# Performance work log

Hardware: AMD Instinct MI355X
Metric: run time of the kernel (lower is better)

Reference implementation:

```python
import jax, jax.numpy as jnp
import numpy as np

N_NODES = 50000
N_EDGES = 800000
IN_DIM, HID_DIM, OUT_DIM, N_HEADS = 256, 256, 64, 4

def setup_inputs() -> dict:
    key = jax.random.key(0)
    ks = jax.random.split(key, 8)
    x = jax.random.normal(ks[0], (N_NODES, IN_DIM), dtype=jnp.float32)
    idx = jax.random.randint(ks[1], (2, N_EDGES), 0, N_NODES, dtype=jnp.int64)
    elem = jax.random.uniform(ks[2], (N_EDGES,), dtype=jnp.float32)
    # MLP params (2 layers: in->hid, hid->out), one set per head; small scale for stability
    W1 = jax.random.normal(ks[3], (N_HEADS, IN_DIM, HID_DIM), dtype=jnp.float32) * 0.05
    b1 = jnp.zeros((N_HEADS, HID_DIM), dtype=jnp.float32)
    W2 = jax.random.normal(ks[4], (N_HEADS, HID_DIM, OUT_DIM), dtype=jnp.float32) * 0.05
    b2 = jnp.zeros((N_HEADS, OUT_DIM), dtype=jnp.float32)
    # Attention: Linear(2*out+1 -> 1)
    attn_w = jax.random.normal(ks[5], (N_HEADS, 2 * OUT_DIM + 1, 1), dtype=jnp.float32) * 0.05
    attn_b = jnp.zeros((N_HEADS, 1), dtype=jnp.float32)
    return {"x": x, "idx": idx, "elem": elem, "W1": W1, "b1": b1,
            "W2": W2, "b2": b2, "attn_w": attn_w, "attn_b": attn_b}

def reference(x, idx, elem, W1, b1, W2, b2, attn_w, attn_b):
    n = x.shape[0]
    src, dst = idx[0], idx[1]

    def head(W1h, b1h, W2h, b2h, awh, abh):
        # 2-layer MLP on node features: [N, out]
        feats = jnp.maximum(x @ W1h + b1h, 0.0) @ W2h + b2h
        f_src = feats[src]            # [E, out]
        f_dst = feats[dst]            # [E, out]
        x_cat = jnp.concatenate([f_src, f_dst, elem[:, None]], axis=1)  # [E, 2*out+1]
        score = (x_cat @ awh + abh)[:, 0]                # [E]
        w = jnp.exp(score - jnp.max(score))              # globally-shifted exp, as in source
        # SpecialSpmm: sparse [N,N] (rows=src, cols=dst, vals=w) @ dense
        pooled = jax.ops.segment_sum(w[:, None] * f_dst, src, num_segments=n)  # [N, out]
        row_sum = jax.ops.segment_sum(w, src, num_segments=n)                  # [N]
        return pooled / row_sum[:, None]

    h = jax.vmap(head)(W1, b1, W2, b2, attn_w, attn_b)   # [H, N, out]
    return jnp.transpose(h, (1, 0, 2)).reshape(n, -1)    # cat heads -> [N, H*out]
```

## Files before the change

### kernel.cpp

```cpp
#include <hip/hip_runtime.h>
#include <math.h>


#define N_HEADS 4
#define IN_DIM 256
#define HID_DIM 256
#define OUT_DIM 64
#define ATT_STRIDE (2 * OUT_DIM + 1)
#define LDSP 264

typedef __attribute__((ext_vector_type(8))) short bf16x8;
typedef __attribute__((ext_vector_type(4))) float f32x4;

__device__ __forceinline__ unsigned short bf16rne(float f) {
  unsigned int u = __float_as_uint(f);
  u += 0x7fffu + ((u >> 16) & 1u);
  return (unsigned short)(u >> 16);
}


#define W1N (N_HEADS * IN_DIM * HID_DIM)
#define W2N (N_HEADS * HID_DIM * OUT_DIM)

__global__ __launch_bounds__(256) void convw_kernel(const float* __restrict__ W1,
                                                    const float* __restrict__ W2,
                                                    unsigned short* __restrict__ W1T,
                                                    unsigned short* __restrict__ W2T) {
  int id = blockIdx.x * 256 + threadIdx.x;
  if (id < W1N) {
    int k = id & 255, j = (id >> 8) & 255, h = id >> 16;
    W1T[id] = bf16rne(W1[((size_t)h * 256 + k) * 256 + j]);
  } else if (id < W1N + W2N) {
    int t = id - W1N;
    int k = t & 255, d = (t >> 8) & 63, h = t >> 14;
    W2T[t] = bf16rne(W2[((size_t)h * 256 + k) * 64 + d]);
  }
}


__global__ __launch_bounds__(256) void count_kernel(const int* __restrict__ src,
                                                    int* __restrict__ cnt, int E) {
  int e = blockIdx.x * 256 + threadIdx.x;
  if (e < E) atomicAdd(&cnt[src[e]], 1);
}

__global__ __launch_bounds__(1024) void scan_kernel(const int* __restrict__ cnt,
                                                    int* __restrict__ offs, int N) {
  __shared__ int part[1024];
  int t = threadIdx.x;
  int chunk = (N + 1023) >> 10;
  int s0 = t * chunk;
  int s1e = min(s0 + chunk, N);
  int sum = 0;
  for (int i = s0; i < s1e; ++i) sum += cnt[i];
  part[t] = sum;
  __syncthreads();
  for (int off = 1; off < 1024; off <<= 1) {
    int v = (t >= off) ? part[t - off] : 0;
    __syncthreads();
    part[t] += v;
    __syncthreads();
  }
  int run = (t == 0) ? 0 : part[t - 1];
  for (int i = s0; i < s1e; ++i) { offs[i] = run; run += cnt[i]; }
  if (t == 0) offs[N] = part[1023];
}

__global__ __launch_bounds__(256) void scatter_kernel(
    const int* __restrict__ src, const int* __restrict__ dst,
    const float* __restrict__ elem, const int* __restrict__ offs,
    int* __restrict__ cur, int* __restrict__ dst2, float* __restrict__ elem2,
    int E) {
  int e = blockIdx.x * 256 + threadIdx.x;
  if (e < E) {
    int s = src[e];
    int pos = offs[s] + atomicAdd(&cur[s], 1);
    dst2[pos] = dst[e];
    elem2[pos] = elem[e];
  }
}


__global__ __launch_bounds__(256) void feats_kernel(
    const float* __restrict__ x, const unsigned short* __restrict__ W1T,
    const float* __restrict__ b1, const unsigned short* __restrict__ W2T,
    const float* __restrict__ b2, const float* __restrict__ attn_w,
    const float* __restrict__ attn_b, float* __restrict__ feats,
    float* __restrict__ s1, float* __restrict__ s2, int N) {
  __shared__ __align__(16) unsigned short xs[64 * LDSP];
  __shared__ __align__(16) unsigned short hs[64 * LDSP];

  int h = blockIdx.y;
  int n0 = blockIdx.x * 64;
  int tid = threadIdx.x;
  int w = tid >> 6, l = tid & 63;
  int lr = l & 15, kb = l >> 4;

#pragma unroll
  for (int i = 0; i < 8; ++i) {
    int flat = i * 2048 + tid * 8;
    int r = flat >> 8, c = flat & 255;
    int n = n0 + r;
    float4 v0 = make_float4(0.f, 0.f, 0.f, 0.f), v1 = v0;
    if (n < N) {
      const float* p = x + (size_t)n * IN_DIM + c;
      v0 = *(const float4*)p;
      v1 = *(const float4*)(p + 4);
    }
    uint4 pk;
    pk.x = (unsigned)bf16rne(v0.x) | ((unsigned)bf16rne(v0.y) << 16);
    pk.y = (unsigned)bf16rne(v0.z) | ((unsigned)bf16rne(v0.w) << 16);
    pk.z = (unsigned)bf16rne(v1.x) | ((unsigned)bf16rne(v1.y) << 16);
    pk.w = (unsigned)bf16rne(v1.z) | ((unsigned)bf16rne(v1.w) << 16);
    *(uint4*)&xs[r * LDSP + c] = pk;
  }
  __syncthreads();

  int j0 = w * 64;
  const unsigned short* W1Th = W1T + (size_t)h * 256 * 256;
  f32x4 acc[4][4];
#pragma unroll
  for (int mi = 0; mi < 4; ++mi)
#pragma unroll
    for (int ni = 0; ni < 4; ++ni) acc[mi][ni] = (f32x4){0.f, 0.f, 0.f, 0.f};

#pragma unroll
  for (int kk = 0; kk < 8; ++kk) {
    int k0 = kk * 32 + kb * 8;
    bf16x8 a[4], b[4];
#pragma unroll
    for (int mi = 0; mi < 4; ++mi)
      a[mi] = *(const bf16x8*)&xs[(mi * 16 + lr) * LDSP + k0];
#pragma unroll
    for (int ni = 0; ni < 4; ++ni)
      b[ni] = *(const bf16x8*)(W1Th + (size_t)(j0 + ni * 16 + lr) * 256 + k0);
#pragma unroll
    for (int mi = 0; mi < 4; ++mi)
#pragma unroll
      for (int ni = 0; ni < 4; ++ni)
        acc[mi][ni] = __builtin_amdgcn_mfma_f32_16x16x32_bf16(a[mi], b[ni],
                                                              acc[mi][ni], 0, 0, 0);
  }

  float b1v[4];
#pragma unroll
  for (int ni = 0; ni < 4; ++ni) b1v[ni] = b1[h * HID_DIM + j0 + ni * 16 + lr];
#pragma unroll
  for (int mi = 0; mi < 4; ++mi)
#pragma unroll
    for (int ni = 0; ni < 4; ++ni)
#pragma unroll
      for (int r = 0; r < 4; ++r) {
        float v = fmaxf(acc[mi][ni][r] + b1v[ni], 0.0f);
        hs[(mi * 16 + kb * 4 + r) * LDSP + (j0 + ni * 16 + lr)] = bf16rne(v);
      }
  __syncthreads();

  const unsigned short* W2Th = W2T + (size_t)h * 64 * 256;
  f32x4 acc2[4];
#pragma unroll
  for (int ni = 0; ni < 4; ++ni) acc2[ni] = (f32x4){0.f, 0.f, 0.f, 0.f};
#pragma unroll
  for (int kk = 0; kk < 8; ++kk) {
    int k0 = kk * 32 + kb * 8;
    bf16x8 a = *(const bf16x8*)&hs[(w * 16 + lr) * LDSP + k0];
#pragma unroll
    for (int ni = 0; ni < 4; ++ni) {
      bf16x8 b = *(const bf16x8*)(W2Th + (size_t)(ni * 16 + lr) * 256 + k0);
      acc2[ni] = __builtin_amdgcn_mfma_f32_16x16x32_bf16(a, b, acc2[ni], 0, 0, 0);
    }
  }

  const float* awh = attn_w + h * ATT_STRIDE;
  float a1v[4], a2v[4], b2v[4];
#pragma unroll
  for (int ni = 0; ni < 4; ++ni) {
    int d = ni * 16 + lr;
    a1v[ni] = awh[d];
    a2v[ni] = awh[OUT_DIM + d];
    b2v[ni] = b2[h * OUT_DIM + d];
  }
#pragma unroll
  for (int r = 0; r < 4; ++r) {
    int n = n0 + w * 16 + kb * 4 + r;
    float vals[4];
    float p1 = 0.f, p2 = 0.f;
#pragma unroll
    for (int ni = 0; ni < 4; ++ni) {
      float v = acc2[ni][r] + b2v[ni];
      vals[ni] = v;
      p1 += v * a1v[ni];
      p2 += v * a2v[ni];
    }
#pragma unroll
    for (int m = 1; m < 16; m <<= 1) {
      p1 += __shfl_xor(p1, m, 64);
      p2 += __shfl_xor(p2, m, 64);
    }
    if (n < N) {
      float* fr = feats + ((size_t)h * N + n) * OUT_DIM;
#pragma unroll
      for (int ni = 0; ni < 4; ++ni) fr[ni * 16 + lr] = vals[ni];
      if (lr == 0) {
        s1[(size_t)h * N + n] = p1;
        s2[(size_t)h * N + n] = p2;
      }
    }
  }
}


__global__ __launch_bounds__(256) void edgemax_kernel(
    const int* __restrict__ src, const int* __restrict__ dst,
    const float* __restrict__ elem, const float* __restrict__ s1,
    const float* __restrict__ s2, const float* __restrict__ attn_w,
    const float* __restrict__ attn_b, float* __restrict__ blockmax, int N, int E) {
  int e = blockIdx.x * 256 + threadIdx.x;
  float sc[N_HEADS];
  if (e < E) {
    int s = src[e], dn = dst[e];
    float el = elem[e];
#pragma unroll
    for (int h = 0; h < N_HEADS; ++h)
      sc[h] = s1[(size_t)h * N + s] + s2[(size_t)h * N + dn] +
              attn_w[h * ATT_STRIDE + 2 * OUT_DIM] * el + attn_b[h];
  } else {
#pragma unroll
    for (int h = 0; h < N_HEADS; ++h) sc[h] = -INFINITY;
  }
  __shared__ float wm[N_HEADS][4];
  int lane = threadIdx.x & 63, wv = threadIdx.x >> 6;
#pragma unroll
  for (int h = 0; h < N_HEADS; ++h) {
    float m = sc[h];
#pragma unroll
    for (int off = 32; off > 0; off >>= 1) m = fmaxf(m, __shfl_down(m, off, 64));
    if (lane == 0) wm[h][wv] = m;
  }
  __syncthreads();
  if (threadIdx.x < N_HEADS) {
    int h = threadIdx.x;
    float m = fmaxf(fmaxf(wm[h][0], wm[h][1]), fmaxf(wm[h][2], wm[h][3]));
    blockmax[blockIdx.x * N_HEADS + h] = m;
  }
}

__global__ __launch_bounds__(256) void reducemax_kernel(
    const float* __restrict__ blockmax, float* __restrict__ maxs, int nb) {
  __shared__ float red[256];
  int tid = threadIdx.x;
  for (int h = 0; h < N_HEADS; ++h) {
    float m = -INFINITY;
    for (int i = tid; i < nb; i += 256) m = fmaxf(m, blockmax[i * N_HEADS + h]);
    red[tid] = m;
    __syncthreads();
    for (int s = 128; s > 0; s >>= 1) {
      if (tid < s) red[tid] = fmaxf(red[tid], red[tid + s]);
      __syncthreads();
    }
    if (tid == 0) maxs[h] = red[0];
    __syncthreads();
  }
}


#define AGG_U 8

__global__ __launch_bounds__(256) void aggregate_kernel(
    const int* __restrict__ dst2, const float* __restrict__ elem2,
    const int* __restrict__ offs, const float* __restrict__ s1,
    const float* __restrict__ s2, const float* __restrict__ feats,
    const float* __restrict__ attn_w, const float* __restrict__ attn_b,
    const float* __restrict__ maxs, float* __restrict__ out, int N) {
  int n = blockIdx.x;
  int h = threadIdx.x >> 6, d = threadIdx.x & 63;
  int beg = offs[n], end = offs[n + 1];
  float s1n = s1[(size_t)h * N + n];
  float awe = attn_w[h * ATT_STRIDE + 2 * OUT_DIM];
  float ab = attn_b[h];
  float mx = maxs[h];
  const float* fh = feats + (size_t)h * N * OUT_DIM;
  const float* s2h = s2 + (size_t)h * N;
  float acc = 0.f, rs = 0.f;
  float base = s1n + ab - mx;

  for (int p = beg; p < end; p += AGG_U) {
    int dn[AGG_U];
    float el[AGG_U];
#pragma unroll
    for (int i = 0; i < AGG_U; ++i) {
      int q = (p + i < end) ? p + i : beg;
      dn[i] = dst2[q];
      el[i] = elem2[q];
    }
    float s2v[AGG_U], fv[AGG_U];
#pragma unroll
    for (int i = 0; i < AGG_U; ++i) s2v[i] = s2h[dn[i]];
#pragma unroll
    for (int i = 0; i < AGG_U; ++i) fv[i] = fh[(size_t)dn[i] * OUT_DIM + d];
#pragma unroll
    for (int i = 0; i < AGG_U; ++i) {
      float wv = (p + i < end) ? __expf(base + s2v[i] + awe * el[i]) : 0.f;
      acc = fmaf(wv, fv[i], acc);
      rs += wv;
    }
  }
  out[(size_t)n * (N_HEADS * OUT_DIM) + h * OUT_DIM + d] = acc / rs;
}


extern "C" void kernel_launch(void* const* d_in, const int* in_sizes, int n_in,
                              void* d_out, int out_size, void* d_ws, size_t ws_size,
                              hipStream_t stream) {
  const float* x = (const float*)d_in[0];
  const int* idx = (const int*)d_in[1];
  const float* elem = (const float*)d_in[2];
  const float* W1 = (const float*)d_in[3];
  const float* b1 = (const float*)d_in[4];
  const float* W2 = (const float*)d_in[5];
  const float* b2 = (const float*)d_in[6];
  const float* attn_w = (const float*)d_in[7];
  const float* attn_b = (const float*)d_in[8];
  float* out = (float*)d_out;

  int N = in_sizes[0] / IN_DIM;
  int E = in_sizes[2];
  const int* src = idx;
  const int* dst = idx + E;
  int nb = (E + 255) / 256;

  unsigned short* W1T = (unsigned short*)d_ws;
  unsigned short* W2T = W1T + W1N;
  float* feats = (float*)(W2T + W2N);
  float* s1 = feats + (size_t)N_HEADS * N * OUT_DIM;
  float* s2 = s1 + (size_t)N_HEADS * N;
  float* blockmax = s2 + (size_t)N_HEADS * N;
  float* maxs = blockmax + (size_t)nb * N_HEADS;
  int* offs = (int*)(maxs + 64);
  int* cur = offs + (N + 64);
  int* dst2 = cur + (N + 64);
  float* elem2 = (float*)(dst2 + E);

  convw_kernel<<<(W1N + W2N + 255) / 256, 256, 0, stream>>>(W1, W2, W1T, W2T);

  hipMemsetAsync(cur, 0, sizeof(int) * (size_t)N, stream);
  count_kernel<<<nb, 256, 0, stream>>>(src, cur, E);
  scan_kernel<<<1, 1024, 0, stream>>>(cur, offs, N);
  hipMemsetAsync(cur, 0, sizeof(int) * (size_t)N, stream);
  scatter_kernel<<<nb, 256, 0, stream>>>(src, dst, elem, offs, cur, dst2, elem2, E);

  dim3 g((N + 63) / 64, N_HEADS);
  feats_kernel<<<g, 256, 0, stream>>>(x, W1T, b1, W2T, b2, attn_w, attn_b,
                                      feats, s1, s2, N);
  edgemax_kernel<<<nb, 256, 0, stream>>>(src, dst, elem, s1, s2, attn_w, attn_b,
                                         blockmax, N, E);
  reducemax_kernel<<<1, 256, 0, stream>>>(blockmax, maxs, nb);
  aggregate_kernel<<<N, 256, 0, stream>>>(dst2, elem2, offs, s1, s2, feats,
                                          attn_w, attn_b, maxs, out, N);
}
```

Baseline: 565.1 us.

## Drop global max pass, store feats in bf16, loop heads per block

Removes the edge max and reduce-max kernels, relying on the cancellation of the global shift in the normalized softmax ratio. It stores node features as bf16 and s1/s2 node-major to halve the gather traffic in aggregation. Aggregation now processes two edges per wave, with each lane handling two feature elements, and combines the halves with a cross-lane shuffle. The feature kernel loops over all heads in one block so the x tile is loaded and converted once. Without the max shift, exp can overflow for large scores, and bf16 features reduce precision.

```diff
diff --git a/kernel.cpp b/kernel.cpp
--- a/kernel.cpp
+++ b/kernel.cpp
@@ -85,12 +85,11 @@
     const float* __restrict__ x, const unsigned short* __restrict__ W1T,
     const float* __restrict__ b1, const unsigned short* __restrict__ W2T,
     const float* __restrict__ b2, const float* __restrict__ attn_w,
-    const float* __restrict__ attn_b, float* __restrict__ feats,
-    float* __restrict__ s1, float* __restrict__ s2, int N) {
+    const float* __restrict__ attn_b, unsigned short* __restrict__ feats_g,
+    float* __restrict__ s1p, float* __restrict__ s2p, int N) {
   __shared__ __align__(16) unsigned short xs[64 * LDSP];
   __shared__ __align__(16) unsigned short hs[64 * LDSP];
 
-  int h = blockIdx.y;
   int n0 = blockIdx.x * 64;
   int tid = threadIdx.x;
   int w = tid >> 6, l = tid & 63;
@@ -117,149 +116,98 @@
   __syncthreads();
 
   int j0 = w * 64;
-  const unsigned short* W1Th = W1T + (size_t)h * 256 * 256;
-  f32x4 acc[4][4];
-#pragma unroll
-  for (int mi = 0; mi < 4; ++mi)
-#pragma unroll
-    for (int ni = 0; ni < 4; ++ni) acc[mi][ni] = (f32x4){0.f, 0.f, 0.f, 0.f};
-
-#pragma unroll
-  for (int kk = 0; kk < 8; ++kk) {
-    int k0 = kk * 32 + kb * 8;
-    bf16x8 a[4], b[4];
+  for (int h = 0; h < N_HEADS; ++h) {
+    const unsigned short* W1Th = W1T + (size_t)h * 256 * 256;
+    f32x4 acc[4][4];
 #pragma unroll
     for (int mi = 0; mi < 4; ++mi)
-      a[mi] = *(const bf16x8*)&xs[(mi * 16 + lr) * LDSP + k0];
-#pragma unroll
-    for (int ni = 0; ni < 4; ++ni)
-      b[ni] = *(const bf16x8*)(W1Th + (size_t)(j0 + ni * 16 + lr) * 256 + k0);
+#pragma unroll
+      for (int ni = 0; ni < 4; ++ni) acc[mi][ni] = (f32x4){0.f, 0.f, 0.f, 0.f};
+
+#pragma unroll
+    for (int kk = 0; kk < 8; ++kk) {
+      int k0 = kk * 32 + kb * 8;
+      bf16x8 a[4], b[4];
+#pragma unroll
+      for (int mi = 0; mi < 4; ++mi)
+        a[mi] = *(const bf16x8*)&xs[(mi * 16 + lr) * LDSP + k0];
+#pragma unroll
+      for (int ni = 0; ni < 4; ++ni)
+        b[ni] = *(const bf16x8*)(W1Th + (size_t)(j0 + ni * 16 + lr) * 256 + k0);
+#pragma unroll
+      for (int mi = 0; mi < 4; ++mi)
+#pragma unroll
+        for (int ni = 0; ni < 4; ++ni)
+          acc[mi][ni] = __builtin_amdgcn_mfma_f32_16x16x32_bf16(a[mi], b[ni],
+                                                                acc[mi][ni], 0, 0, 0);
+    }
+
+    float b1v[4];
+#pragma unroll
+    for (int ni = 0; ni < 4; ++ni) b1v[ni] = b1[h * HID_DIM + j0 + ni * 16 + lr];
+    __syncthreads();
 #pragma unroll
     for (int mi = 0; mi < 4; ++mi)
 #pragma unroll
       for (int ni = 0; ni < 4; ++ni)
-        acc[mi][ni] = __builtin_amdgcn_mfma_f32_16x16x32_bf16(a[mi], b[ni],
-                                                              acc[mi][ni], 0, 0, 0);
-  }
-
-  float b1v[4];
-#pragma unroll
-  for (int ni = 0; ni < 4; ++ni) b1v[ni] = b1[h * HID_DIM + j0 + ni * 16 + lr];
-#pragma unroll
-  for (int mi = 0; mi < 4; ++mi)
-#pragma unroll
-    for (int ni = 0; ni < 4; ++ni)
-#pragma unroll
-      for (int r = 0; r < 4; ++r) {
-        float v = fmaxf(acc[mi][ni][r] + b1v[ni], 0.0f);
-        hs[(mi * 16 + kb * 4 + r) * LDSP + (j0 + ni * 16 + lr)] = bf16rne(v);
+#pragma unroll
+        for (int r = 0; r < 4; ++r) {
+          float v = fmaxf(acc[mi][ni][r] + b1v[ni], 0.0f);
+          hs[(mi * 16 + kb * 4 + r) * LDSP + (j0 + ni * 16 + lr)] = bf16rne(v);
+        }
+    __syncthreads();
+
+    const unsigned short* W2Th = W2T + (size_t)h * 64 * 256;
+    f32x4 acc2[4];
+#pragma unroll
+    for (int ni = 0; ni < 4; ++ni) acc2[ni] = (f32x4){0.f, 0.f, 0.f, 0.f};
+#pragma unroll
+    for (int kk = 0; kk < 8; ++kk) {
+      int k0 = kk * 32 + kb * 8;
+      bf16x8 a = *(const bf16x8*)&hs[(w * 16 + lr) * LDSP + k0];
+#pragma unroll
+      for (int ni = 0; ni < 4; ++ni) {
+        bf16x8 b = *(const bf16x8*)(W2Th + (size_t)(ni * 16 + lr) * 256 + k0);
+        acc2[ni] = __builtin_amdgcn_mfma_f32_16x16x32_bf16(a, b, acc2[ni], 0, 0, 0);
       }
-  __syncthreads();
-
-  const unsigned short* W2Th = W2T + (size_t)h * 64 * 256;
-  f32x4 acc2[4];
-#pragma unroll
-  for (int ni = 0; ni < 4; ++ni) acc2[ni] = (f32x4){0.f, 0.f, 0.f, 0.f};
-#pragma unroll
-  for (int kk = 0; kk < 8; ++kk) {
-    int k0 = kk * 32 + kb * 8;
-    bf16x8 a = *(const bf16x8*)&hs[(w * 16 + lr) * LDSP + k0];
+    }
+
+    const float* awh = attn_w + h * ATT_STRIDE;
+    float a1v[4], a2v[4], b2v[4];
 #pragma unroll
     for (int ni = 0; ni < 4; ++ni) {
-      bf16x8 b = *(const bf16x8*)(W2Th + (size_t)(ni * 16 + lr) * 256 + k0);
-      acc2[ni] = __builtin_amdgcn_mfma_f32_16x16x32_bf16(a, b, acc2[ni], 0, 0, 0);
-    }
-  }
-
-  const float* awh = attn_w + h * ATT_STRIDE;
-  float a1v[4], a2v[4], b2v[4];
-#pragma unroll
-  for (int ni = 0; ni < 4; ++ni) {
-    int d = ni * 16 + lr;
-    a1v[ni] = awh[d];
-    a2v[ni] = awh[OUT_DIM + d];
-    b2v[ni] = b2[h * OUT_DIM + d];
-  }
-#pragma unroll
-  for (int r = 0; r < 4; ++r) {
-    int n = n0 + w * 16 + kb * 4 + r;
-    float vals[4];
-    float p1 = 0.f, p2 = 0.f;
-#pragma unroll
-    for (int ni = 0; ni < 4; ++ni) {
-      float v = acc2[ni][r] + b2v[ni];
-      vals[ni] = v;
-      p1 += v * a1v[ni];
-      p2 += v * a2v[ni];
-    }
-#pragma unroll
-    for (int m = 1; m < 16; m <<= 1) {
-      p1 += __shfl_xor(p1, m, 64);
-      p2 += __shfl_xor(p2, m, 64);
-    }
-    if (n < N) {
-      float* fr = feats + ((size_t)h * N + n) * OUT_DIM;
-#pragma unroll
-      for (int ni = 0; ni < 4; ++ni) fr[ni * 16 + lr] = vals[ni];
-      if (lr == 0) {
-        s1[(size_t)h * N + n] = p1;
-        s2[(size_t)h * N + n] = p2;
+      int d = ni * 16 + lr;
+      a1v[ni] = awh[d];
+      a2v[ni] = awh[OUT_DIM + d];
+      b2v[ni] = b2[h * OUT_DIM + d];
+    }
+#pragma unroll
+    for (int r = 0; r < 4; ++r) {
+      int n = n0 + w * 16 + kb * 4 + r;
+      float vals[4];
+      float p1 = 0.f, p2 = 0.f;
+#pragma unroll
+      for (int ni = 0; ni < 4; ++ni) {
+        float v = acc2[ni][r] + b2v[ni];
+        vals[ni] = v;
+        p1 += v * a1v[ni];
+        p2 += v * a2v[ni];
       }
-    }
-  }
-}
-
-
-__global__ __launch_bounds__(256) void edgemax_kernel(
-    const int* __restrict__ src, const int* __restrict__ dst,
-    const float* __restrict__ elem, const float* __restrict__ s1,
-    const float* __restrict__ s2, const float* __restrict__ attn_w,
-    const float* __restrict__ attn_b, float* __restrict__ blockmax, int N, int E) {
-  int e = blockIdx.x * 256 + threadIdx.x;
-  float sc[N_HEADS];
-  if (e < E) {
-    int s = src[e], dn = dst[e];
-    float el = elem[e];
-#pragma unroll
-    for (int h = 0; h < N_HEADS; ++h)
-      sc[h] = s1[(size_t)h * N + s] + s2[(size_t)h * N + dn] +
-              attn_w[h * ATT_STRIDE + 2 * OUT_DIM] * el + attn_b[h];
-  } else {
-#pragma unroll
-    for (int h = 0; h < N_HEADS; ++h) sc[h] = -INFINITY;
-  }
-  __shared__ float wm[N_HEADS][4];
-  int lane = threadIdx.x & 63, wv = threadIdx.x >> 6;
-#pragma unroll
-  for (int h = 0; h < N_HEADS; ++h) {
-    float m = sc[h];
-#pragma unroll
-    for (int off = 32; off > 0; off >>= 1) m = fmaxf(m, __shfl_down(m, off, 64));
-    if (lane == 0) wm[h][wv] = m;
-  }
-  __syncthreads();
-  if (threadIdx.x < N_HEADS) {
-    int h = threadIdx.x;
-    float m = fmaxf(fmaxf(wm[h][0], wm[h][1]), fmaxf(wm[h][2], wm[h][3]));
-    blockmax[blockIdx.x * N_HEADS + h] = m;
-  }
-}
-
-__global__ __launch_bounds__(256) void reducemax_kernel(
-    const float* __restrict__ blockmax, float* __restrict__ maxs, int nb) {
-  __shared__ float red[256];
-  int tid = threadIdx.x;
-  for (int h = 0; h < N_HEADS; ++h) {
-    float m = -INFINITY;
-    for (int i = tid; i < nb; i += 256) m = fmaxf(m, blockmax[i * N_HEADS + h]);
-    red[tid] = m;
-    __syncthreads();
-    for (int s = 128; s > 0; s >>= 1) {
-      if (tid < s) red[tid] = fmaxf(red[tid], red[tid + s]);
-      __syncthreads();
-    }
-    if (tid == 0) maxs[h] = red[0];
-    __syncthreads();
+#pragma unroll
+      for (int m = 1; m < 16; m <<= 1) {
+        p1 += __shfl_xor(p1, m, 64);
+        p2 += __shfl_xor(p2, m, 64);
+      }
+      if (n < N) {
+        unsigned short* fr = feats_g + ((size_t)h * N + n) * OUT_DIM;
+#pragma unroll
+        for (int ni = 0; ni < 4; ++ni) fr[ni * 16 + lr] = bf16rne(vals[ni]);
+        if (lr == 0) {
+          s1p[(size_t)n * N_HEADS + h] = p1;
+          s2p[(size_t)n * N_HEADS + h] = p2;
+        }
+      }
+    }
   }
 }
 
@@ -268,44 +216,55 @@
 
 __global__ __launch_bounds__(256) void aggregate_kernel(
     const int* __restrict__ dst2, const float* __restrict__ elem2,
-    const int* __restrict__ offs, const float* __restrict__ s1,
-    const float* __restrict__ s2, const float* __restrict__ feats,
+    const int* __restrict__ offs, const float* __restrict__ s1p,
+    const float* __restrict__ s2p, const unsigned short* __restrict__ feats_g,
     const float* __restrict__ attn_w, const float* __restrict__ attn_b,
-    const float* __restrict__ maxs, float* __restrict__ out, int N) {
+    float* __restrict__ out, int N) {
   int n = blockIdx.x;
-  int h = threadIdx.x >> 6, d = threadIdx.x & 63;
+  int h = threadIdx.x >> 6;
+  int l = threadIdx.x & 63;
+  int j = l >> 5, dp = l & 31;
   int beg = offs[n], end = offs[n + 1];
-  float s1n = s1[(size_t)h * N + n];
+  float base = s1p[(size_t)n * N_HEADS + h] + attn_b[h];
   float awe = attn_w[h * ATT_STRIDE + 2 * OUT_DIM];
-  float ab = attn_b[h];
-  float mx = maxs[h];
-  const float* fh = feats + (size_t)h * N * OUT_DIM;
-  const float* s2h = s2 + (size_t)h * N;
-  float acc = 0.f, rs = 0.f;
-  float base = s1n + ab - mx;
-
-  for (int p = beg; p < end; p += AGG_U) {
+  const unsigned short* fg = feats_g + (size_t)h * N * OUT_DIM;
+  float acc0 = 0.f, acc1 = 0.f, rs = 0.f;
+
+  for (int p = beg; p < end; p += 2 * AGG_U) {
     int dn[AGG_U];
     float el[AGG_U];
 #pragma unroll
     for (int i = 0; i < AGG_U; ++i) {
-      int q = (p + i < end) ? p + i : beg;
-      dn[i] = dst2[q];
-      el[i] = elem2[q];
-    }
-    float s2v[AGG_U], fv[AGG_U];
-#pragma unroll
-    for (int i = 0; i < AGG_U; ++i) s2v[i] = s2h[dn[i]];
-#pragma unroll
-    for (int i = 0; i < AGG_U; ++i) fv[i] = fh[(size_t)dn[i] * OUT_DIM + d];
+      int q = p + 2 * i + j;
+      int qq = (q < end) ? q : beg;
+      dn[i] = dst2[qq];
+      el[i] = elem2[qq];
+    }
+    float s2v[AGG_U];
+    unsigned int fv[AGG_U];
+#pragma unroll
+    for (int i = 0; i < AGG_U; ++i) s2v[i] = s2p[(size_t)dn[i] * N_HEADS + h];
+#pragma unroll
+    for (int i = 0; i < AGG_U; ++i)
+      fv[i] = *(const unsigned int*)&fg[(size_t)dn[i] * OUT_DIM + 2 * dp];
 #pragma unroll
     for (int i = 0; i < AGG_U; ++i) {
-      float wv = (p + i < end) ? __expf(base + s2v[i] + awe * el[i]) : 0.f;
-      acc = fmaf(wv, fv[i], acc);
+      float wv = (p + 2 * i + j < end) ? __expf(base + s2v[i] + awe * el[i]) : 0.f;
+      float f0 = __uint_as_float(fv[i] << 16);
+      float f1 = __uint_as_float(fv[i] & 0xffff0000u);
+      acc0 = fmaf(wv, f0, acc0);
+      acc1 = fmaf(wv, f1, acc1);
       rs += wv;
     }
   }
-  out[(size_t)n * (N_HEADS * OUT_DIM) + h * OUT_DIM + d] = acc / rs;
+  acc0 += __shfl_xor(acc0, 32, 64);
+  acc1 += __shfl_xor(acc1, 32, 64);
+  rs += __shfl_xor(rs, 32, 64);
+  if (j == 0) {
+    float inv = 1.0f / rs;
+    float2 o = make_float2(acc0 * inv, acc1 * inv);
+    *(float2*)&out[(size_t)n * (N_HEADS * OUT_DIM) + h * OUT_DIM + 2 * dp] = o;
+  }
 }
 
 
@@ -331,12 +290,10 @@
 
   unsigned short* W1T = (unsigned short*)d_ws;
   unsigned short* W2T = W1T + W1N;
-  float* feats = (float*)(W2T + W2N);
-  float* s1 = feats + (size_t)N_HEADS * N * OUT_DIM;
-  float* s2 = s1 + (size_t)N_HEADS * N;
-  float* blockmax = s2 + (size_t)N_HEADS * N;
-  float* maxs = blockmax + (size_t)nb * N_HEADS;
-  int* offs = (int*)(maxs + 64);
+  unsigned short* feats_g = W2T + W2N;
+  float* s1p = (float*)(feats_g + (size_t)N_HEADS * N * OUT_DIM);
+  float* s2p = s1p + (size_t)N * N_HEADS;
+  int* offs = (int*)(s2p + (size_t)N * N_HEADS);
   int* cur = offs + (N + 64);
   int* dst2 = cur + (N + 64);
   float* elem2 = (float*)(dst2 + E);
@@ -349,12 +306,8 @@
   hipMemsetAsync(cur, 0, sizeof(int) * (size_t)N, stream);
   scatter_kernel<<<nb, 256, 0, stream>>>(src, dst, elem, offs, cur, dst2, elem2, E);
 
-  dim3 g((N + 63) / 64, N_HEADS);
-  feats_kernel<<<g, 256, 0, stream>>>(x, W1T, b1, W2T, b2, attn_w, attn_b,
-                                      feats, s1, s2, N);
-  edgemax_kernel<<<nb, 256, 0, stream>>>(src, dst, elem, s1, s2, attn_w, attn_b,
-                                         blockmax, N, E);
-  reducemax_kernel<<<1, 256, 0, stream>>>(blockmax, maxs, nb);
-  aggregate_kernel<<<N, 256, 0, stream>>>(dst2, elem2, offs, s1, s2, feats,
-                                          attn_w, attn_b, maxs, out, N);
-}
+  feats_kernel<<<(N + 63) / 64, 256, 0, stream>>>(x, W1T, b1, W2T, b2, attn_w,
+                                                  attn_b, feats_g, s1p, s2p, N);
+  aggregate_kernel<<<N, 256, 0, stream>>>(dst2, elem2, offs, s1p, s2p, feats_g,
+                                          attn_w, attn_b, out, N);
+}
```

Result: faster. 499.9 us (-11.5%).
